# Kernel optimization log

Hardware: AMD Instinct MI355X
Metric: run time of the kernel (lower is better)

The kernel has to match this reference:

```python
import jax, jax.numpy as jnp
import numpy as np

N_NODES = 100000
N_EDGES = 3200000
IN_DIM, HID, OUT_DIM = 1, 64, 1


def graph_conv(x, src, dst, ew, W_rel, b_rel, W_root):
    # PyG GraphConv (aggr='add'): out_i = W_rel @ sum_{j->i} w_ij x_j + b_rel + W_root @ x_i
    msg = x[src] * ew[:, None]                               # [E, F]
    agg = jax.ops.segment_sum(msg, dst, num_segments=N_NODES)  # [N, F]
    return agg @ W_rel + b_rel + x @ W_root


def setup_inputs() -> dict:
    key = jax.random.key(0)
    ks = jax.random.split(key, 12)
    def glorot(k, shape):
        fan_in, fan_out = shape
        lim = float(np.sqrt(6.0 / (fan_in + fan_out)))
        return jax.random.uniform(k, shape, jnp.float32, -lim, lim)
    x = jax.random.normal(ks[0], (N_NODES, IN_DIM), jnp.float32)
    edge_index = jax.random.randint(ks[1], (2, N_EDGES), 0, N_NODES, jnp.int64)
    edge_weight = jax.random.uniform(ks[2], (N_EDGES,), jnp.float32)
    return {
        "x": x, "edge_index": edge_index, "edge_weight": edge_weight,
        "W1_rel": glorot(ks[3], (IN_DIM, HID)), "b1": jnp.zeros((HID,), jnp.float32),
        "W1_root": glorot(ks[4], (IN_DIM, HID)),
        "W2_rel": glorot(ks[5], (HID, HID)), "b2": jnp.zeros((HID,), jnp.float32),
        "W2_root": glorot(ks[6], (HID, HID)),
        "W3_rel": glorot(ks[7], (HID, OUT_DIM)), "b3": jnp.zeros((OUT_DIM,), jnp.float32),
        "W3_root": glorot(ks[8], (HID, OUT_DIM)),
    }


def reference(x, edge_index, edge_weight, W1_rel, b1, W1_root, W2_rel, b2, W2_root, W3_rel, b3, W3_root):
    src, dst = edge_index[0], edge_index[1]
    h = graph_conv(x, src, dst, edge_weight, W1_rel, b1, W1_root)
    h = jax.nn.relu(h)  # dropout is identity in eval mode
    h = graph_conv(h, src, dst, edge_weight, W2_rel, b2, W2_root)
    h = jax.nn.relu(h)
    return graph_conv(h, src, dst, edge_weight, W3_rel, b3, W3_root)
```

## Files before the change

### kernel.cpp

```cpp
#include <hip/hip_runtime.h>

#define NN 100000
#define NE 3200000
#define HID 64
#define NPB 256
#define NB  ((NN + NPB - 1) / NPB)
#define NNP (NB * NPB)
#define CAP 9216
#define MNP 128
#define NMW (2 * NB)
#define CAPW 5120
#define CHUNK 4096
#define NCH ((NE + CHUNK - 1) / CHUNK)
#define AP 72
#define BPITCH 136
#define SRCM 0x1FFFF

typedef _Float16 half8 __attribute__((ext_vector_type(8)));
typedef _Float16 h2v   __attribute__((ext_vector_type(2)));
typedef float f32x4 __attribute__((ext_vector_type(4)));

__device__ __forceinline__ unsigned short f2hb(float v) {
    _Float16 h = (_Float16)v;
    unsigned short s;
    __builtin_memcpy(&s, &h, 2);
    return s;
}
__device__ __forceinline__ float h2f(unsigned int u) {
    unsigned short s = (unsigned short)u;
    _Float16 h;
    __builtin_memcpy(&h, &s, 2);
    return (float)h;
}
__device__ __forceinline__ h2v ash2(unsigned int u) {
    h2v r;
    __builtin_memcpy(&r, &u, 4);
    return r;
}

__global__ __launch_bounds__(512) void k_init(const float* __restrict__ x,
                                              float2* __restrict__ sx,
                                              int* __restrict__ gcur) {
    const int i = blockIdx.x * 512 + threadIdx.x;
    if (i < NN) sx[i] = make_float2(0.f, x[i]);
    if (blockIdx.x == 0 && threadIdx.x < NB) gcur[threadIdx.x] = threadIdx.x * CAP;
}

__global__ __launch_bounds__(512) void k_scatter(const int* __restrict__ src,
                                                 const int* __restrict__ dst,
                                                 const float* __restrict__ ew,
                                                 int* __restrict__ gcur,
                                                 int* __restrict__ rec_a,
                                                 unsigned short* __restrict__ rec_w) {
    __shared__ int la[CHUNK];
    __shared__ unsigned short lw[CHUNK];
    __shared__ unsigned short lb[CHUNK];
    __shared__ unsigned short sidx[CHUNK];
    __shared__ int cnt[NB];
    __shared__ int bme[NB];
    __shared__ int wt8[8];
    const int tid = threadIdx.x;
    const int lane = tid & 63, wvx = tid >> 6;
    for (int j = tid; j < NB; j += 512) cnt[j] = 0;
    __syncthreads();
    const long long b0 = (long long)blockIdx.x * CHUNK;
    const int valid = (int)min((long long)CHUNK, (long long)NE - b0);
    #pragma unroll
    for (int k = 0; k < CHUNK / 512; ++k) {
        int idx = k * 512 + tid;
        if (idx < valid) {
            long long e = b0 + idx;
            int d = dst[e];
            int b = d >> 8;
            la[idx] = src[e] | ((d & 255) << 17);
            lw[idx] = f2hb(ew[e]);
            lb[idx] = (unsigned short)b;
            atomicAdd(&cnt[b], 1);
        }
    }
    __syncthreads();
    const int v = (tid < NB) ? cnt[tid] : 0;
    int incl = v;
    #pragma unroll
    for (int off = 1; off < 64; off <<= 1) {
        int t0 = __shfl_up(incl, off, 64);
        if (lane >= off) incl += t0;
    }
    if (lane == 63) wt8[wvx] = incl;
    __syncthreads();
    int offs = 0;
    #pragma unroll
    for (int j = 0; j < 8; ++j)
        if (j < wvx) offs += wt8[j];
    const int excl = offs + incl - v;
    if (tid < NB) {
        int bb = v ? atomicAdd(&gcur[tid], v) : 0;
        bme[tid] = bb - excl;
        cnt[tid] = excl;
    }
    __syncthreads();
    #pragma unroll
    for (int k = 0; k < CHUNK / 512; ++k) {
        int idx = k * 512 + tid;
        if (idx < valid) {
            int sp = atomicAdd(&cnt[lb[idx]], 1);
            sidx[sp] = (unsigned short)idx;
        }
    }
    __syncthreads();
    #pragma unroll
    for (int k = 0; k < CHUNK / 512; ++k) {
        int sp = k * 512 + tid;
        if (sp < valid) {
            int idx = sidx[sp];
            int b = lb[idx];
            int go = bme[b] + sp;
            rec_a[go] = la[idx];
            rec_w[go] = lw[idx];
        }
    }
}

__global__ __launch_bounds__(512) void k_s1(const int* __restrict__ gcur,
                                            const int* __restrict__ rec_a,
                                            const unsigned short* __restrict__ rec_w,
                                            const float* __restrict__ x,
                                            float* __restrict__ sxf) {
    __shared__ float loc[NPB];
    if (threadIdx.x < NPB) loc[threadIdx.x] = 0.f;
    __syncthreads();
    const int wid = blockIdx.x;
    const int b = wid >> 2, j = wid & 3;
    const int beg = b * CAP, cnt = gcur[b] - beg;
    const int qtr = (cnt + 3) >> 2;
    const int s0 = beg + min(cnt, j * qtr);
    const int s1e = beg + min(cnt, (j + 1) * qtr);
    for (int t = s0 + threadIdx.x; t < s1e; t += 512) {
        const int a = rec_a[t];
        const float w = h2f(rec_w[t]);
        atomicAdd(&loc[a >> 17], w * x[a & SRCM]);
    }
    __syncthreads();
    const int i = b * NPB + threadIdx.x;
    if (threadIdx.x < NPB && i < NN) {
        float v = loc[threadIdx.x];
        if (v != 0.f) atomicAdd(&sxf[2 * i], v);
    }
}

__global__ __launch_bounds__(512) void k_pack(const int* __restrict__ gcur,
                                              const int* __restrict__ rec_a,
                                              const unsigned short* __restrict__ rec_w,
                                              const float2* __restrict__ sx,
                                              unsigned short* __restrict__ rec2s,
                                              unsigned short* __restrict__ rec2x,
                                              unsigned short* __restrict__ rec2f,
                                              int* __restrict__ noff,
                                              unsigned char* __restrict__ ngrp) {
    __shared__ int4 imgq[3 * CAPW / 8];
    __shared__ int hist[128];
    __shared__ int exclp[128];
    __shared__ int cur[128];
    __shared__ int wt2[2];
    unsigned short* img = (unsigned short*)imgq;
    unsigned short* ws_img = img;
    unsigned short* wx_img = img + CAPW;
    unsigned short* wf_img = img + 2 * CAPW;
    const int tid = threadIdx.x;
    const int lane = tid & 63, wv = tid >> 6;
    const int wid = blockIdx.x;
    const int b = wid >> 1, h = wid & 1;
    for (int j = tid; j < 3 * CAPW / 8; j += 512) imgq[j] = (int4){0, 0, 0, 0};
    if (tid < 128) hist[tid] = 0;
    __syncthreads();
    const int beg = b * CAP;
    const int cnt = gcur[b] - beg;
    {
        const int4* a4 = (const int4*)(rec_a + beg);
        const int n4 = cnt >> 2;
        for (int t = tid; t < n4; t += 512) {
            int4 q = a4[t];
            int d0 = q.x >> 17, d1 = q.y >> 17, d2 = q.z >> 17, d3 = q.w >> 17;
            if ((d0 >> 7) == h) atomicAdd(&hist[d0 & 127], 1);
            if ((d1 >> 7) == h) atomicAdd(&hist[d1 & 127], 1);
            if ((d2 >> 7) == h) atomicAdd(&hist[d2 & 127], 1);
            if ((d3 >> 7) == h) atomicAdd(&hist[d3 & 127], 1);
        }
        for (int t = (n4 << 2) + tid; t < cnt; t += 512) {
            int dl = rec_a[beg + t] >> 17;
            if ((dl >> 7) == h) atomicAdd(&hist[dl & 127], 1);
        }
    }
    __syncthreads();
    int pc = 0, incl = 0;
    if (tid < 128) { pc = (hist[tid] + 7) & ~7; incl = pc; }
    #pragma unroll
    for (int off = 1; off < 64; off <<= 1) {
        int tt = __shfl_up(incl, off, 64);
        if (lane >= off) incl += tt;
    }
    if (tid < 128 && lane == 63) wt2[wv] = incl;
    __syncthreads();
    if (tid < 128) {
        int e0 = ((tid >= 64) ? wt2[0] : 0) + incl - pc;
        exclp[tid] = e0;
        cur[tid] = e0;
        const int node = wid * MNP + tid;
        noff[node] = wid * CAPW + e0;
        ngrp[node] = (unsigned char)(pc >> 3);
    }
    __syncthreads();
#define PREC(AA, WW) {                                                  \
        const int dl_ = (AA) >> 17;                                     \
        if ((dl_ >> 7) == h) {                                          \
            const float w_ = h2f(WW);                                   \
            const float2 v_ = sx[(AA) & SRCM];                          \
            int gs_ = atomicAdd(&cur[dl_ & 127], 1);                    \
            ws_img[gs_] = f2hb(w_ * v_.x);                              \
            wx_img[gs_] = f2hb(w_ * v_.y);                              \
            wf_img[gs_] = (unsigned short)(WW);                         \
        } }
    {
        const int4* a4 = (const int4*)(rec_a + beg);
        const ushort4* w4 = (const ushort4*)(rec_w + beg);
        const int n4 = cnt >> 2;
        for (int t = tid; t < n4; t += 512) {
            int4 qa = a4[t];
            ushort4 qw = w4[t];
            PREC(qa.x, qw.x)
            PREC(qa.y, qw.y)
            PREC(qa.z, qw.z)
            PREC(qa.w, qw.w)
        }
        for (int t = (n4 << 2) + tid; t < cnt; t += 512) {
            PREC(rec_a[beg + t], rec_w[beg + t])
        }
    }
#undef PREC
    __syncthreads();
    {
        const size_t pb = (size_t)wid * (CAPW / 8);
        int4* d0 = (int4*)rec2s + pb;
        int4* d1 = (int4*)rec2x + pb;
        int4* d2 = (int4*)rec2f + pb;
        for (int j = tid; j < CAPW / 8; j += 512) d0[j] = imgq[j];
        for (int j = tid; j < CAPW / 8; j += 512) d1[j] = imgq[CAPW / 8 + j];
        for (int j = tid; j < CAPW / 8; j += 512) d2[j] = imgq[2 * (CAPW / 8) + j];
    }
}

__global__ __launch_bounds__(512) void k_mega(
        const int* __restrict__ noff, const unsigned char* __restrict__ ngrp,
        const unsigned short* __restrict__ rec2s,
        const unsigned short* __restrict__ rec2x,
        const unsigned short* __restrict__ rec2f,
        const float2* __restrict__ sx,
        const float* __restrict__ W1_rel, const float* __restrict__ W1_root,
        const float* __restrict__ b1,
        const float* __restrict__ W2_rel, const float* __restrict__ b2,
        const float* __restrict__ W2_root,
        const float* __restrict__ W3_rel, const float* __restrict__ W3_root,
        const float* __restrict__ b3,
        float* __restrict__ p, float* __restrict__ out) {
    __shared__ _Float16 aggh[MNP * AP];
    __shared__ _Float16 Bt[HID * BPITCH];
    __shared__ float2 sxl[MNP];
    const int tid = threadIdx.x;
    const int f = tid & 63;
    const int wv = tid >> 6;
    const int gi0 = blockIdx.x * MNP;

    for (int j = tid; j < MNP * AP / 2; j += 512) ((int*)aggh)[j] = 0;
    for (int idx = tid; idx < HID * HID; idx += 512) {
        int k = idx >> 6, n = idx & 63;
        Bt[n * BPITCH + k]       = (_Float16)W2_rel[idx];
        Bt[n * BPITCH + HID + k] = (_Float16)W2_root[idx];
    }
    if (tid < MNP) {
        int gi = gi0 + tid;
        sxl[tid] = (gi < NN) ? sx[gi] : make_float2(0.f, 0.f);
    }
    const float w1rf = W1_rel[f], w1tf = W1_root[f], b1ff = b1[f];
    const float b3v = b3[0];
    __syncthreads();

    {
        const int first = gi0 + wv * 16;
        int soff = __builtin_amdgcn_readfirstlane(noff[first]);
        const int4 gvv = *(const int4*)(ngrp + first);
        unsigned ua = __builtin_amdgcn_readfirstlane((unsigned)gvv.x);
        unsigned ub = __builtin_amdgcn_readfirstlane((unsigned)gvv.y);
        unsigned uc = __builtin_amdgcn_readfirstlane((unsigned)gvv.z);
        unsigned ud = __builtin_amdgcn_readfirstlane((unsigned)gvv.w);
        unsigned long long clo = (unsigned long long)ua | ((unsigned long long)ub << 32);
        unsigned long long chi = (unsigned long long)uc | ((unsigned long long)ud << 32);
        #define BSUM(u) (((u) & 255u) + (((u) >> 8) & 255u) + (((u) >> 16) & 255u) + ((u) >> 24))
        const int tg = (int)(BSUM(ua) + BSUM(ub) + BSUM(uc) + BSUM(ud));
        #undef BSUM

        const h2v w1r2 = {(_Float16)w1rf, (_Float16)w1rf};
        const h2v w1t2 = {(_Float16)w1tf, (_Float16)w1tf};
        const h2v b1f2 = {(_Float16)b1ff, (_Float16)b1ff};
        const h2v one2 = {(_Float16)1.f, (_Float16)1.f};
        const h2v zero2 = {(_Float16)0.f, (_Float16)0.f};

        float a0 = 0.f, a1 = 0.f, a2 = 0.f, a3 = 0.f;
        int nrow = wv * 16;
        const int rowend = nrow + 16;
        int grem = (int)(clo & 255); clo = (clo >> 8) | (chi << 56); chi >>= 8;
        while (grem == 0 && nrow + 1 < rowend) {
            ++nrow; grem = (int)(clo & 255);
            clo = (clo >> 8) | (chi << 56); chi >>= 8;
        }

        const int4* ps = (const int4*)rec2s + (soff >> 3);
        const int4* px = (const int4*)rec2x + (soff >> 3);
        const int4* pf = (const int4*)rec2f + (soff >> 3);

        int4 S0, X0, F0, S1, X1, F1, S2, X2, F2, S3, X3, F3;
        if (tg >= 1) { S0 = ps[0]; X0 = px[0]; F0 = pf[0]; }
        if (tg >= 2) { S1 = ps[1]; X1 = px[1]; F1 = pf[1]; }
        if (tg >= 3) { S2 = ps[2]; X2 = px[2]; F2 = pf[2]; }

#define PP(SS, XX, FF, AA) {                                 \
        h2v z_ = ash2((unsigned)(FF)) * b1f2;                \
        z_ = ash2((unsigned)(XX)) * w1t2 + z_;               \
        z_ = ash2((unsigned)(SS)) * w1r2 + z_;               \
        z_ = __builtin_elementwise_max(z_, zero2);           \
        AA = __builtin_amdgcn_fdot2(z_, one2, AA, false); }

#define GRP(S, X, F)                                         \
        PP(S.x, X.x, F.x, a0) PP(S.y, X.y, F.y, a1)          \
        PP(S.z, X.z, F.z, a2) PP(S.w, X.w, F.w, a3)

#define BNDRY() {                                                        \
        if (--grem == 0) {                                               \
            aggh[nrow * AP + f] = (_Float16)((a0 + a1) + (a2 + a3));     \
            a0 = a1 = a2 = a3 = 0.f;                                     \
            ++nrow; grem = (int)(clo & 255);                             \
            clo = (clo >> 8) | (chi << 56); chi >>= 8;                   \
            while (grem == 0 && nrow + 1 < rowend) {                     \
                ++nrow; grem = (int)(clo & 255);                         \
                clo = (clo >> 8) | (chi << 56); chi >>= 8;               \
            }                                                            \
        } }

        int t = 0;
        while (t + 4 <= tg) {
            S3 = ps[t + 3]; X3 = px[t + 3]; F3 = pf[t + 3];
            GRP(S0, X0, F0) BNDRY(); ++t;
            S0 = ps[t + 3]; X0 = px[t + 3]; F0 = pf[t + 3];
            GRP(S1, X1, F1) BNDRY(); ++t;
            S1 = ps[t + 3]; X1 = px[t + 3]; F1 = pf[t + 3];
            GRP(S2, X2, F2) BNDRY(); ++t;
            S2 = ps[t + 3]; X2 = px[t + 3]; F2 = pf[t + 3];
            GRP(S3, X3, F3) BNDRY(); ++t;
        }
        if (t < tg) {
            GRP(S0, X0, F0) BNDRY(); ++t;
            if (t < tg) {
                GRP(S1, X1, F1) BNDRY(); ++t;
                if (t < tg) {
                    GRP(S2, X2, F2) BNDRY(); ++t;
                }
            }
        }
#undef PP
#undef GRP
#undef BNDRY
    }
    __syncthreads();

    const int m16 = tid & 15;
    const int quad = (tid & 63) >> 4;
    f32x4 acc[4];
    #pragma unroll
    for (int c_ = 0; c_ < 4; ++c_) acc[c_] = (f32x4){0.f, 0.f, 0.f, 0.f};

    const float2 sm = sxl[wv * 16 + m16];

    #pragma unroll
    for (int kt = 0; kt < 4; ++kt) {
        const int kk = kt * 32;
        half8 af;
        if (kt < 2) {
            af = *(const half8*)&aggh[(wv * 16 + m16) * AP + kk + quad * 8];
        } else {
            const int fk0 = (kt - 2) * 32 + quad * 8;
            #pragma unroll
            for (int j = 0; j < 8; ++j) {
                const float wr = W1_rel[fk0 + j], wt = W1_root[fk0 + j], bb = b1[fk0 + j];
                af[j] = (_Float16)fmaxf(0.f, fmaf(sm.x, wr, fmaf(sm.y, wt, bb)));
            }
        }
        #pragma unroll
        for (int ct = 0; ct < 4; ++ct) {
            const half8 bfrag = *(const half8*)&Bt[(ct * 16 + m16) * BPITCH + kk + quad * 8];
            acc[ct] = __builtin_amdgcn_mfma_f32_16x16x32_f16(af, bfrag, acc[ct], 0, 0, 0);
        }
    }

    float b2c[4], w3rc[4], w3tc[4];
    #pragma unroll
    for (int ct = 0; ct < 4; ++ct) {
        const int col = ct * 16 + m16;
        b2c[ct] = b2[col]; w3rc[ct] = W3_rel[col]; w3tc[ct] = W3_root[col];
    }
    float pv[4] = {0.f, 0.f, 0.f, 0.f}, rv[4] = {0.f, 0.f, 0.f, 0.f};
    #pragma unroll
    for (int ct = 0; ct < 4; ++ct) {
        #pragma unroll
        for (int reg = 0; reg < 4; ++reg) {
            const float h2_ = fmaxf(0.f, acc[ct][reg] + b2c[ct]);
            pv[reg] = fmaf(h2_, w3rc[ct], pv[reg]);
            rv[reg] = fmaf(h2_, w3tc[ct], rv[reg]);
        }
    }
    #pragma unroll
    for (int reg = 0; reg < 4; ++reg) {
        #pragma unroll
        for (int msk = 1; msk < 16; msk <<= 1) {
            pv[reg] += __shfl_xor(pv[reg], msk, 64);
            rv[reg] += __shfl_xor(rv[reg], msk, 64);
        }
    }
    if (m16 == 0) {
        #pragma unroll
        for (int reg = 0; reg < 4; ++reg) {
            const int gi = gi0 + wv * 16 + quad * 4 + reg;
            if (gi < NN) { p[gi] = pv[reg]; out[gi] = rv[reg] + b3v; }
        }
    }
}

__global__ __launch_bounds__(512) void k_out(const int* __restrict__ gcur,
                                             const int* __restrict__ rec_a,
                                             const unsigned short* __restrict__ rec_w,
                                             const float* __restrict__ pp,
                                             float* __restrict__ out) {
    __shared__ float loc[NPB];
    if (threadIdx.x < NPB) loc[threadIdx.x] = 0.f;
    __syncthreads();
    const int wid = blockIdx.x;
    const int b = wid >> 2, j = wid & 3;
    const int beg = b * CAP, cnt = gcur[b] - beg;
    const int qtr = (cnt + 3) >> 2;
    const int s0 = beg + min(cnt, j * qtr);
    const int s1e = beg + min(cnt, (j + 1) * qtr);
    for (int t = s0 + threadIdx.x; t < s1e; t += 512) {
        const int a = rec_a[t];
        const float w = h2f(rec_w[t]);
        atomicAdd(&loc[a >> 17], w * pp[a & SRCM]);
    }
    __syncthreads();
    const int i = b * NPB + threadIdx.x;
    if (threadIdx.x < NPB && i < NN) {
        float v = loc[threadIdx.x];
        if (v != 0.f) atomicAdd(&out[i], v);
    }
}

extern "C" void kernel_launch(void* const* d_in, const int* in_sizes, int n_in,
                              void* d_out, int out_size, void* d_ws, size_t ws_size,
                              hipStream_t stream) {
    const float* x       = (const float*)d_in[0];
    const int*   ei      = (const int*)  d_in[1];
    const float* ew      = (const float*)d_in[2];
    const float* W1_rel  = (const float*)d_in[3];
    const float* b1      = (const float*)d_in[4];
    const float* W1_root = (const float*)d_in[5];
    const float* W2_rel  = (const float*)d_in[6];
    const float* b2      = (const float*)d_in[7];
    const float* W2_root = (const float*)d_in[8];
    const float* W3_rel  = (const float*)d_in[9];
    const float* b3      = (const float*)d_in[10];
    const float* W3_root = (const float*)d_in[11];

    const int* src = ei;
    const int* dst = ei + NE;

    const size_t REC_SLOTS = (size_t)NB * CAP;
    const size_t PLANE     = (size_t)NMW * CAPW;
    int*            rec_a = (int*)d_ws;
    unsigned short* rec_w = (unsigned short*)(rec_a + REC_SLOTS);
    float2*         sx    = (float2*)(rec_w + REC_SLOTS);
    float*          p     = (float*)(sx + NN);
    int*            noff  = (int*)(p + NN);
    unsigned char*  ngrp  = (unsigned char*)(noff + NNP);
    int*            gcur  = (int*)(ngrp + NNP);
    char*           tail  = (char*)(gcur + NB);
    size_t          off   = ((size_t)(tail - (char*)d_ws) + 15) & ~(size_t)15;
    unsigned short* rec2s = (unsigned short*)((char*)d_ws + off);
    unsigned short* rec2x = rec2s + PLANE;
    unsigned short* rec2f = rec2x + PLANE;

    k_init<<<(NN + 511) / 512, 512, 0, stream>>>(x, sx, gcur);
    k_scatter<<<NCH, 512, 0, stream>>>(src, dst, ew, gcur, rec_a, rec_w);
    k_s1<<<4 * NB, 512, 0, stream>>>(gcur, rec_a, rec_w, x, (float*)sx);
    k_pack<<<NMW, 512, 0, stream>>>(gcur, rec_a, rec_w, sx,
                                    rec2s, rec2x, rec2f, noff, ngrp);
    k_mega<<<NMW, 512, 0, stream>>>(noff, ngrp, rec2s, rec2x, rec2f, sx,
                                    W1_rel, W1_root, b1,
                                    W2_rel, b2, W2_root,
                                    W3_rel, W3_root, b3, p, (float*)d_out);
    k_out<<<4 * NB, 512, 0, stream>>>(gcur, rec_a, rec_w, p, (float*)d_out);
}
```

Measured before the change: 237.3 us.

## Halve nodes per k_mega block and split MFMA columns across wave pairs

k_mega now processes 64 nodes per block instead of 128, launching twice as many blocks. Each wave aggregates 8 node rows instead of 16. In the MFMA stage, the 8 waves form a 4x2 grid over rows and column tiles, and the two column-half partial sums are combined through shared memory. The aim is more parallelism and better load balance for the latency-bound gather phase, at the cost of an extra barrier, extra shared reductions and duplicated per-block weight staging.

```diff
diff --git a/kernel.cpp b/kernel.cpp
--- a/kernel.cpp
+++ b/kernel.cpp
@@ -9,6 +9,8 @@
 #define CAP 9216
 #define MNP 128
 #define NMW (2 * NB)
+#define WNP 64
+#define NW2 (NNP / WNP)
 #define CAPW 5120
 #define CHUNK 4096
 #define NCH ((NE + CHUNK - 1) / CHUNK)
@@ -262,21 +264,23 @@
         const float* __restrict__ W3_rel, const float* __restrict__ W3_root,
         const float* __restrict__ b3,
         float* __restrict__ p, float* __restrict__ out) {
-    __shared__ _Float16 aggh[MNP * AP];
+    __shared__ _Float16 aggh[WNP * AP];
     __shared__ _Float16 Bt[HID * BPITCH];
-    __shared__ float2 sxl[MNP];
+    __shared__ float2 sxl[WNP];
+    __shared__ float partP[2][WNP];
+    __shared__ float partR[2][WNP];
     const int tid = threadIdx.x;
     const int f = tid & 63;
     const int wv = tid >> 6;
-    const int gi0 = blockIdx.x * MNP;
-
-    for (int j = tid; j < MNP * AP / 2; j += 512) ((int*)aggh)[j] = 0;
+    const int gi0 = blockIdx.x * WNP;
+
+    for (int j = tid; j < WNP * AP / 2; j += 512) ((int*)aggh)[j] = 0;
     for (int idx = tid; idx < HID * HID; idx += 512) {
         int k = idx >> 6, n = idx & 63;
         Bt[n * BPITCH + k]       = (_Float16)W2_rel[idx];
         Bt[n * BPITCH + HID + k] = (_Float16)W2_root[idx];
     }
-    if (tid < MNP) {
+    if (tid < WNP) {
         int gi = gi0 + tid;
         sxl[tid] = (gi < NN) ? sx[gi] : make_float2(0.f, 0.f);
     }
@@ -285,17 +289,14 @@
     __syncthreads();
 
     {
-        const int first = gi0 + wv * 16;
+        const int first = gi0 + wv * 8;
         int soff = __builtin_amdgcn_readfirstlane(noff[first]);
-        const int4 gvv = *(const int4*)(ngrp + first);
-        unsigned ua = __builtin_amdgcn_readfirstlane((unsigned)gvv.x);
-        unsigned ub = __builtin_amdgcn_readfirstlane((unsigned)gvv.y);
-        unsigned uc = __builtin_amdgcn_readfirstlane((unsigned)gvv.z);
-        unsigned ud = __builtin_amdgcn_readfirstlane((unsigned)gvv.w);
+        const int2 gv = *(const int2*)(ngrp + first);
+        unsigned ua = __builtin_amdgcn_readfirstlane((unsigned)gv.x);
+        unsigned ub = __builtin_amdgcn_readfirstlane((unsigned)gv.y);
         unsigned long long clo = (unsigned long long)ua | ((unsigned long long)ub << 32);
-        unsigned long long chi = (unsigned long long)uc | ((unsigned long long)ud << 32);
         #define BSUM(u) (((u) & 255u) + (((u) >> 8) & 255u) + (((u) >> 16) & 255u) + ((u) >> 24))
-        const int tg = (int)(BSUM(ua) + BSUM(ub) + BSUM(uc) + BSUM(ud));
+        const int tg = (int)(BSUM(ua) + BSUM(ub));
         #undef BSUM
 
         const h2v w1r2 = {(_Float16)w1rf, (_Float16)w1rf};
@@ -305,12 +306,11 @@
         const h2v zero2 = {(_Float16)0.f, (_Float16)0.f};
 
         float a0 = 0.f, a1 = 0.f, a2 = 0.f, a3 = 0.f;
-        int nrow = wv * 16;
-        const int rowend = nrow + 16;
-        int grem = (int)(clo & 255); clo = (clo >> 8) | (chi << 56); chi >>= 8;
+        int nrow = wv * 8;
+        const int rowend = nrow + 8;
+        int grem = (int)(clo & 255); clo >>= 8;
         while (grem == 0 && nrow + 1 < rowend) {
-            ++nrow; grem = (int)(clo & 255);
-            clo = (clo >> 8) | (chi << 56); chi >>= 8;
+            ++nrow; grem = (int)(clo & 255); clo >>= 8;
         }
 
         const int4* ps = (const int4*)rec2s + (soff >> 3);
@@ -337,11 +337,9 @@
         if (--grem == 0) {                                               \
             aggh[nrow * AP + f] = (_Float16)((a0 + a1) + (a2 + a3));     \
             a0 = a1 = a2 = a3 = 0.f;                                     \
-            ++nrow; grem = (int)(clo & 255);                             \
-            clo = (clo >> 8) | (chi << 56); chi >>= 8;                   \
+            ++nrow; grem = (int)(clo & 255); clo >>= 8;                  \
             while (grem == 0 && nrow + 1 < rowend) {                     \
-                ++nrow; grem = (int)(clo & 255);                         \
-                clo = (clo >> 8) | (chi << 56); chi >>= 8;               \
+                ++nrow; grem = (int)(clo & 255); clo >>= 8;              \
             }                                                            \
         } }
 
@@ -373,18 +371,20 @@
 
     const int m16 = tid & 15;
     const int quad = (tid & 63) >> 4;
-    f32x4 acc[4];
-    #pragma unroll
-    for (int c_ = 0; c_ < 4; ++c_) acc[c_] = (f32x4){0.f, 0.f, 0.f, 0.f};
-
-    const float2 sm = sxl[wv * 16 + m16];
+    const int rw = wv & 3;
+    const int cw = wv >> 2;
+    f32x4 acc[2];
+    acc[0] = (f32x4){0.f, 0.f, 0.f, 0.f};
+    acc[1] = (f32x4){0.f, 0.f, 0.f, 0.f};
+
+    const float2 sm = sxl[rw * 16 + m16];
 
     #pragma unroll
     for (int kt = 0; kt < 4; ++kt) {
         const int kk = kt * 32;
         half8 af;
         if (kt < 2) {
-            af = *(const half8*)&aggh[(wv * 16 + m16) * AP + kk + quad * 8];
+            af = *(const half8*)&aggh[(rw * 16 + m16) * AP + kk + quad * 8];
         } else {
             const int fk0 = (kt - 2) * 32 + quad * 8;
             #pragma unroll
@@ -394,26 +394,27 @@
             }
         }
         #pragma unroll
-        for (int ct = 0; ct < 4; ++ct) {
+        for (int c = 0; c < 2; ++c) {
+            const int ct = cw * 2 + c;
             const half8 bfrag = *(const half8*)&Bt[(ct * 16 + m16) * BPITCH + kk + quad * 8];
-            acc[ct] = __builtin_amdgcn_mfma_f32_16x16x32_f16(af, bfrag, acc[ct], 0, 0, 0);
-        }
-    }
-
-    float b2c[4], w3rc[4], w3tc[4];
-    #pragma unroll
-    for (int ct = 0; ct < 4; ++ct) {
-        const int col = ct * 16 + m16;
-        b2c[ct] = b2[col]; w3rc[ct] = W3_rel[col]; w3tc[ct] = W3_root[col];
+            acc[c] = __builtin_amdgcn_mfma_f32_16x16x32_f16(af, bfrag, acc[c], 0, 0, 0);
+        }
+    }
+
+    float b2c[2], w3rc[2], w3tc[2];
+    #pragma unroll
+    for (int c = 0; c < 2; ++c) {
+        const int col = (cw * 2 + c) * 16 + m16;
+        b2c[c] = b2[col]; w3rc[c] = W3_rel[col]; w3tc[c] = W3_root[col];
     }
     float pv[4] = {0.f, 0.f, 0.f, 0.f}, rv[4] = {0.f, 0.f, 0.f, 0.f};
     #pragma unroll
-    for (int ct = 0; ct < 4; ++ct) {
+    for (int c = 0; c < 2; ++c) {
         #pragma unroll
         for (int reg = 0; reg < 4; ++reg) {
-            const float h2_ = fmaxf(0.f, acc[ct][reg] + b2c[ct]);
-            pv[reg] = fmaf(h2_, w3rc[ct], pv[reg]);
-            rv[reg] = fmaf(h2_, w3tc[ct], rv[reg]);
+            const float h2_ = fmaxf(0.f, acc[c][reg] + b2c[c]);
+            pv[reg] = fmaf(h2_, w3rc[c], pv[reg]);
+            rv[reg] = fmaf(h2_, w3tc[c], rv[reg]);
         }
     }
     #pragma unroll
@@ -427,8 +428,17 @@
     if (m16 == 0) {
         #pragma unroll
         for (int reg = 0; reg < 4; ++reg) {
-            const int gi = gi0 + wv * 16 + quad * 4 + reg;
-            if (gi < NN) { p[gi] = pv[reg]; out[gi] = rv[reg] + b3v; }
+            const int row = rw * 16 + quad * 4 + reg;
+            partP[cw][row] = pv[reg];
+            partR[cw][row] = rv[reg];
+        }
+    }
+    __syncthreads();
+    if (tid < WNP) {
+        const int gi = gi0 + tid;
+        if (gi < NN) {
+            p[gi]   = partP[0][tid] + partP[1][tid];
+            out[gi] = partR[0][tid] + partR[1][tid] + b3v;
         }
     }
 }
@@ -499,7 +509,7 @@
     k_s1<<<4 * NB, 512, 0, stream>>>(gcur, rec_a, rec_w, x, (float*)sx);
     k_pack<<<NMW, 512, 0, stream>>>(gcur, rec_a, rec_w, sx,
                                     rec2s, rec2x, rec2f, noff, ngrp);
-    k_mega<<<NMW, 512, 0, stream>>>(noff, ngrp, rec2s, rec2x, rec2f, sx,
+    k_mega<<<NW2, 512, 0, stream>>>(noff, ngrp, rec2s, rec2x, rec2f, sx,
                                     W1_rel, W1_root, b1,
                                     W2_rel, b2, W2_root,
                                     W3_rel, W3_root, b3, p, (float*)d_out);
```

Result: no change. 234.5 us (-1.2%).
